# Optimization experiments

Hardware: AMD Instinct MI355X
Metric: run time of the kernel (lower is better)

The kernel has to match this reference:

```python
import jax, jax.numpy as jnp
import numpy as np

HID = 512
B, T, INP_DIM, ACT_DIM = 16, 1000, 4, 1
DT = 0.01  # t_const


def _masks(hid, dtype=jnp.float32):
    q, half, k = hid // 4, hid // 2, int(0.3 * hid)
    strthal = jnp.concatenate([jnp.zeros(q), jnp.ones(half), jnp.zeros(q), jnp.zeros(5 * hid)]).astype(dtype)
    tonic = jnp.concatenate([jnp.zeros(hid), jnp.ones(2 * hid), jnp.zeros(hid), jnp.ones(hid), jnp.zeros(hid)]).astype(dtype)
    alm_mask = jnp.concatenate([jnp.zeros(5 * hid), jnp.ones(hid)]).astype(dtype)
    alm2str_m = jnp.concatenate([jnp.ones((hid, hid - k)), jnp.zeros((hid, k))], axis=1).astype(dtype)
    thal2str_m = jnp.concatenate([jnp.zeros((q, hid)), jnp.ones((half, hid)), jnp.zeros((q, hid))], axis=0).astype(dtype)
    str2snr_m = jnp.concatenate([jnp.ones((hid, half)), jnp.zeros((hid, half))], axis=1).astype(dtype)
    str2gpe_m = jnp.concatenate([jnp.zeros((hid, half)), jnp.ones((hid, half))], axis=1).astype(dtype)
    alm_d = jnp.ones(hid, dtype).at[hid - k:].set(-1.0)  # diag of alm2alm_D
    return strthal, tonic, alm_mask, alm2str_m, thal2str_m, str2snr_m, str2gpe_m, alm_d


def _forward(inp, hn, x, inhib_stim, str2str_w, thal2alm_w, thal2str_w, alm2alm_w,
             alm2str_w, str2snr_w, str2gpe_w, gpe2stn_w, stn2snr_w, snr2thal_w,
             inp_weight, fc1, fc2, str2str_fixed):
    hid = str2str_w.shape[0]
    strthal, tonic, alm_mask, alm2str_m, thal2str_m, str2snr_m, str2gpe_m, alm_d = _masks(hid, inp.dtype)
    relu = jax.nn.relu
    # region-to-region effective weights (D matrices are (+/-) identity -> sign/col scale)
    str2str = -str2str_fixed              # str2str_mask is all zeros; D = -I
    alm2alm = relu(alm2alm_w) * alm_d[None, :]
    alm2str = alm2str_m * relu(alm2str_w)
    thal2alm = relu(thal2alm_w)
    thal2str = thal2str_m * relu(thal2str_w)
    str2snr = -(str2snr_m * relu(str2snr_w))
    str2gpe = -(str2gpe_m * relu(str2gpe_w))
    gpe2stn = -relu(gpe2stn_w)
    stn2snr = relu(stn2snr_w)
    snr2thal = -relu(snr2thal_w)
    H6 = 6 * hid
    W = jnp.zeros((H6, H6), inp.dtype)
    def blk(W, r, c, m):
        return W.at[r * hid:(r + 1) * hid, c * hid:(c + 1) * hid].set(m)
    # rows: str, gpe, stn, snr, thal, alm
    W = blk(W, 0, 0, str2str); W = blk(W, 0, 4, thal2str); W = blk(W, 0, 5, alm2str)
    W = blk(W, 1, 0, str2gpe)
    W = blk(W, 2, 1, gpe2stn)
    W = blk(W, 3, 0, str2snr); W = blk(W, 3, 2, stn2snr)
    W = blk(W, 4, 3, snr2thal)
    W = blk(W, 5, 4, thal2alm); W = blk(W, 5, 5, alm2alm)
    # precompute per-step external drive (noise=False path)
    drive = jnp.einsum('bti,ih->bth', inp, relu(inp_weight)) * strthal \
            + inhib_stim[:, None, :] + tonic  # [B,T,6h]
    def step(h, d_t):
        h_new = jax.nn.relu(h + DT * (-h + h @ W.T + d_t))
        return h_new, h_new
    h0 = hn[0]
    _, hs = jax.lax.scan(step, h0, jnp.swapaxes(drive, 0, 1))  # [T,B,6h]
    rnn_out = jnp.swapaxes(hs, 0, 1)                           # [B,T,6h]
    x_out = jnp.broadcast_to(x[0][:, None, :], rnn_out.shape)  # x is never updated
    hn_last = rnn_out[:, -1, :][None]
    x_last = x_out[:, -1, :][None]
    out = jax.nn.sigmoid((rnn_out * alm_mask) @ jax.nn.relu(fc1) @ jax.nn.relu(fc2))
    return out, hn_last, rnn_out, x_last, x_out


def setup_inputs() -> dict:
    key = jax.random.key(0)
    ks = jax.random.split(key, 17)
    u = lambda k, shape, hi: jax.random.uniform(k, shape, jnp.float32, 0.0, hi)
    hid = HID
    d = {
        'inp': jax.random.normal(ks[0], (B, T, INP_DIM), jnp.float32),
        'hn': jnp.zeros((1, B, 6 * hid), jnp.float32),
        'x': jnp.zeros((1, B, 6 * hid), jnp.float32),
        'inhib_stim': jnp.zeros((B, 6 * hid), jnp.float32),
        'str2str_w': u(ks[1], (hid, hid), 0.01),
        'thal2alm_w': u(ks[2], (hid, hid), 0.01),
        'thal2str_w': u(ks[3], (hid, hid), 0.01),
        'alm2alm_w': u(ks[4], (hid, hid), 0.01),
        'alm2str_w': u(ks[5], (hid, hid), 0.01),
        'str2snr_w': u(ks[6], (hid, hid), 0.01),
        'str2gpe_w': u(ks[7], (hid, hid), 0.01),
        'gpe2stn_w': u(ks[8], (hid, hid), 0.01),
        'stn2snr_w': u(ks[9], (hid, hid), 0.01),
        'snr2thal_w': u(ks[10], (hid, hid), 0.01),
        'inp_weight': u(ks[11], (INP_DIM, 6 * hid), 0.1),
        'fc1': u(ks[12], (6 * hid, hid), 0.01),
        'fc2': u(ks[13], (hid, ACT_DIM), 0.01),
    }
    sparse_mask = (jax.random.uniform(ks[14], (hid, hid)) < 0.1).astype(jnp.float32)
    d['str2str_fixed'] = u(ks[15], (hid, hid), 0.001) * sparse_mask
    return d


def reference(inp, hn, x, inhib_stim, str2str_w, thal2alm_w, thal2str_w, alm2alm_w,
              alm2str_w, str2snr_w, str2gpe_w, gpe2stn_w, stn2snr_w, snr2thal_w,
              inp_weight, fc1, fc2, str2str_fixed):
    return _forward(inp, hn, x, inhib_stim, str2str_w, thal2alm_w, thal2str_w,
                    alm2alm_w, alm2str_w, str2snr_w, str2gpe_w, gpe2stn_w,
                    stn2snr_w, snr2thal_w, inp_weight, fc1, fc2, str2str_fixed)
```

## Files before the change

kernel.cpp:

```cpp
#include <hip/hip_runtime.h>

#define H6   3072
#define TT   1000
#define NWG  192
#define NTHR 256

typedef short bf16x8 __attribute__((ext_vector_type(8)));
typedef float f32x4  __attribute__((ext_vector_type(4)));
typedef unsigned int u32x4 __attribute__((ext_vector_type(4)));

#define TAG64 0x8000800080008000ull

__device__ __forceinline__ unsigned short f2bf(float f) {
  unsigned u = __float_as_uint(f);
  return (unsigned short)((u + 0x7fffu + ((u >> 16) & 1u)) >> 16);
}
__device__ __forceinline__ float bf2f(unsigned short s) {
  return __uint_as_float(((unsigned)s) << 16);
}

#define WS_WLO 5242880
#define WS_RING 10485760
#define WS_FCV 12058624


__global__ void prep_kernel(
    const float* __restrict__ hn, const float* __restrict__ fixed_,
    const float* __restrict__ thal2alm_w, const float* __restrict__ thal2str_w,
    const float* __restrict__ alm2alm_w, const float* __restrict__ alm2str_w,
    const float* __restrict__ str2snr_w, const float* __restrict__ str2gpe_w,
    const float* __restrict__ gpe2stn_w, const float* __restrict__ stn2snr_w,
    const float* __restrict__ snr2thal_w,
    const float* __restrict__ fc1, const float* __restrict__ fc2,
    unsigned short* __restrict__ Whi, unsigned short* __restrict__ Wlo,
    unsigned short* __restrict__ ring, float* __restrict__ fc_vec)
{
  int gid = blockIdx.x * blockDim.x + threadIdx.x;
  int stride = gridDim.x * blockDim.x;
  const int nbt[6]  = {3,1,1,2,1,2};
  const int woff[6] = {0,786432,1048576,1310720,1835008,2097152};
  for (int idx = gid; idx < 2621440; idx += stride) {
    int u = idx >> 18;
    int t = (u<3)?0:((u<4)?1:((u<5)?2:((u<7)?3:((u<8)?4:5))));
    int local = idx - woff[t];
    int ktot = nbt[t] << 9;
    int j  = local / ktot;
    int kx = local - j*ktot;
    int bi = kx >> 9, kk = kx & 511;
    int src = j*512 + kk;
    float w;
    if (t == 0) {
      if (bi == 0)      w = -fixed_[src];
      else if (bi == 1) w = (j >= 128 && j < 384) ? fmaxf(thal2str_w[src],0.f) : 0.f;
      else              w = (kk < 359) ? fmaxf(alm2str_w[src],0.f) : 0.f;
    } else if (t == 1)  w = (kk >= 256) ? -fmaxf(str2gpe_w[src],0.f) : 0.f;
    else if (t == 2)    w = -fmaxf(gpe2stn_w[src],0.f);
    else if (t == 3)    w = (bi == 0) ? ((kk < 256) ? -fmaxf(str2snr_w[src],0.f) : 0.f)
                                      : fmaxf(stn2snr_w[src],0.f);
    else if (t == 4)    w = -fmaxf(snr2thal_w[src],0.f);
    else                w = (bi == 0) ? fmaxf(thal2alm_w[src],0.f)
                                      : fmaxf(alm2alm_w[src],0.f) * ((kk < 359) ? 1.f : -1.f);
    unsigned short hi = f2bf(w);
    Whi[idx] = hi;
    Wlo[idx] = f2bf(w - bf2f(hi));
  }
  for (int u = gid; u < 7*98304; u += stride)
    ring[u] = (u & 1) ? (unsigned short)0x0000 : (unsigned short)0x8000;
  for (int v = gid; v < 49152; v += stride) {
    int r    = v >> 13;
    int rem  = v & 8191;
    int q    = rem >> 9;
    int rem2 = rem & 511;
    int b    = rem2 >> 5;
    int ko   = rem2 & 31;
    int j    = (r << 9) + (q << 5) + ko;
    float val = hn[b * H6 + j];
    unsigned uh = __float_as_uint(val) >> 16;
    float lof = val - __uint_as_float(uh << 16);
    unsigned ul = __float_as_uint(lof) >> 16;
    int off = r*16384 + q*1024 + b*64 + ((ko>>3)<<4) + (ko & 7);
    ring[7*98304 + off]     = (unsigned short)(uh | 0x8000u);
    ring[7*98304 + off + 8] = (unsigned short)(ul | 0x8000u);
  }
  int wid = gid >> 6, lane = gid & 63;
  if (wid < 512) {
    float s = 0.f;
    for (int m = lane; m < 512; m += 64)
      s += fmaxf(fc1[(2560 + wid)*512 + m], 0.f) * fmaxf(fc2[m], 0.f);
    for (int off = 32; off; off >>= 1) s += __shfl_down(s, off);
    if (lane == 0) fc_vec[wid] = s;
  }
}

template<int NB>
__device__ __forceinline__ void scan_body(
    const float* __restrict__ inp, const float* __restrict__ hn,
    const float* __restrict__ inhib, const float* __restrict__ inp_weight,
    const unsigned short* __restrict__ Whi_g, const unsigned short* __restrict__ Wlo_g,
    unsigned short* __restrict__ ring, float* __restrict__ rnn_out,
    float* red, int type, int tile, int kb0, int kb1, int kb2, int woff)
{
  constexpr int NCW = NB * 4;
  const int tid = threadIdx.x, lane = tid & 63, wave = tid >> 6;
  const int ktot = NB << 9;
  const int jb_local = tile << 4;
  const int jb_glob  = (type << 9) + jb_local;
  const int row = lane & 15, quad = lane >> 4;

  bf16x8 wh[NCW], wl[NCW];
  int coff[NCW];
  {
    const unsigned short* sh = Whi_g + woff + (jb_local + row) * ktot + (quad << 3);
    const unsigned short* sl = Wlo_g + woff + (jb_local + row) * ktot + (quad << 3);
    #pragma unroll
    for (int c = 0; c < NCW; ++c) {
      int gc = wave * NCW + c;
      wh[c] = *(const bf16x8*)(sh + (gc << 5));
      wl[c] = *(const bf16x8*)(sl + (gc << 5));
      int bi = gc >> 4;
      int kbv = (bi == 0) ? kb0 : ((bi == 1) ? kb1 : kb2);
      coff[c] = kbv*32768 + (gc & 15)*2048 + row*128 + quad*32;
    }
  }
  #pragma unroll
  for (int c = 0; c < NCW; ++c)
    asm volatile("" : "+v"(wh[c]), "+v"(wl[c]));

  const int b_ep = row;
  const bool has_inp = (type == 0) && (jb_local >= 128) && (jb_local < 384);
  const int jg0 = jb_glob + (quad << 2);
  const int jl0 = jb_local + (quad << 2);
  const int qs = jl0 >> 5, kos = jl0 & 31;
  const int st_off = type*32768 + qs*2048 + b_ep*128 + ((kos>>3)<<5) + ((kos&7)<<1);
  float hprev[4], dbase[4], iw[4][4];
  #pragma unroll
  for (int r = 0; r < 4; ++r) {
    int jgr = jg0 + r;
    hprev[r] = hn[b_ep * H6 + jgr];
    float tn = ((jgr >= 512 && jgr < 1536) || (jgr >= 2048 && jgr < 2560)) ? 1.f : 0.f;
    dbase[r] = inhib[b_ep * H6 + jgr] + tn;
    #pragma unroll
    for (int i = 0; i < 4; ++i)
      iw[r][i] = has_inp ? fmaxf(inp_weight[i * H6 + jgr], 0.f) : 0.f;
  }

  for (int t = 0; t < TT; ++t) {
    const int s_rd = (t + 7) & 7;
    const char* slotp = (const char*)ring + s_rd * 196608;
    const unsigned e32 = ((((t - 1) >> 3) & 1) ? 0x80008000u : 0u);

    float4 xi = {0.f, 0.f, 0.f, 0.f};
    if (wave == 0 && has_inp) xi = *(const float4*)(inp + (b_ep * TT + t) * 4);

    u32x4 Bhi[NCW], Blo[NCW];
    unsigned todo = (NCW == 12) ? 0xFFFu : ((NCW == 8) ? 0xFFu : 0xFu);
    for (;;) {
      #pragma unroll
      for (int c = 0; c < NCW; ++c) if ((todo >> c) & 1u) {
        const char* pc = slotp + coff[c];
        asm volatile("global_load_dwordx4 %0, %2, off sc0 sc1\n\t"
                     "global_load_dwordx4 %1, %2, off offset:16 sc0 sc1"
                     : "=&v"(Bhi[c]), "=&v"(Blo[c]) : "v"(pc) : "memory");
      }
      asm volatile("s_waitcnt vmcnt(0)" ::: "memory");
      __builtin_amdgcn_sched_barrier(0);
      unsigned nt = 0;
      #pragma unroll
      for (int c = 0; c < NCW; ++c) if ((todo >> c) & 1u) {
        unsigned bad = ((Bhi[c][0] ^ e32) | (Bhi[c][1] ^ e32) |
                        (Bhi[c][2] ^ e32) | (Bhi[c][3] ^ e32) |
                        (Blo[c][0] ^ e32) | (Blo[c][1] ^ e32) |
                        (Blo[c][2] ^ e32) | (Blo[c][3] ^ e32)) & 0x80008000u;
        if (__any(bad != 0u)) nt |= 1u << c;
      }
      if (nt == 0) break;
      todo = nt;
      __builtin_amdgcn_s_sleep(1);
    }
    #pragma unroll
    for (int c = 0; c < NCW; ++c) {
      Bhi[c] &= 0x7fff7fffu;
      Blo[c] &= 0x7fff7fffu;
    }

    f32x4 acc0 = {0,0,0,0}, acc1 = {0,0,0,0}, acc2 = {0,0,0,0};
    #pragma unroll
    for (int c = 0; c < NCW; ++c) {
      bf16x8 hb = __builtin_bit_cast(bf16x8, Bhi[c]);
      bf16x8 lb = __builtin_bit_cast(bf16x8, Blo[c]);
      acc0 = __builtin_amdgcn_mfma_f32_16x16x32_bf16(wh[c], hb, acc0, 0, 0, 0);
      acc1 = __builtin_amdgcn_mfma_f32_16x16x32_bf16(wh[c], lb, acc1, 0, 0, 0);
      acc2 = __builtin_amdgcn_mfma_f32_16x16x32_bf16(wl[c], hb, acc2, 0, 0, 0);
    }
    f32x4 acc = acc0 + acc1 + acc2;

    float* bank = red + (t & 1) * 768;
    if (wave) *(f32x4*)(bank + ((wave - 1) * 64 + lane) * 4) = acc;
    __syncthreads();
    if (wave == 0) {
      acc = acc + *(const f32x4*)(bank + lane * 4)
                + *(const f32x4*)(bank + (64 + lane) * 4)
                + *(const f32x4*)(bank + (128 + lane) * 4);
      float proj[4] = {0.f, 0.f, 0.f, 0.f};
      if (has_inp) {
        #pragma unroll
        for (int r = 0; r < 4; ++r)
          proj[r] = xi.x*iw[r][0] + xi.y*iw[r][1] + xi.z*iw[r][2] + xi.w*iw[r][3];
      }
      const unsigned long long ptag = ((t >> 3) & 1) ? TAG64 : 0ull;
      float4 hv4;
      unsigned long long ph = 0ull, pl = 0ull;
      #pragma unroll
      for (int r = 0; r < 4; ++r) {
        float pre = hprev[r] + 0.01f * (acc[r] + dbase[r] + proj[r] - hprev[r]);
        float hv = fmaxf(pre, 0.f);
        hprev[r] = hv;
        ((float*)&hv4)[r] = hv;
        unsigned uh = __float_as_uint(hv) >> 16;
        float lof = hv - __uint_as_float(uh << 16);
        unsigned ul = __float_as_uint(lof) >> 16;
        ph |= ((unsigned long long)uh) << (16 * r);
        pl |= ((unsigned long long)ul) << (16 * r);
      }
      ph |= ptag; pl |= ptag;
      char* outb = (char*)ring + (t & 7) * 196608 + st_off;
      __hip_atomic_store((unsigned long long*)outb, ph,
                         __ATOMIC_RELAXED, __HIP_MEMORY_SCOPE_AGENT);
      __hip_atomic_store((unsigned long long*)(outb + 16), pl,
                         __ATOMIC_RELAXED, __HIP_MEMORY_SCOPE_AGENT);
      *(float4*)(rnn_out + (size_t)(b_ep * TT + t) * H6 + jg0) = hv4;
    }
  }
}

__global__ void __launch_bounds__(NTHR, 1) scan_kernel(
    const float* __restrict__ inp, const float* __restrict__ hn,
    const float* __restrict__ inhib, const float* __restrict__ inp_weight,
    const unsigned short* __restrict__ Whi_g, const unsigned short* __restrict__ Wlo_g,
    unsigned short* __restrict__ ring, float* __restrict__ rnn_out)
{
  __shared__ float red[2 * 768];
  int wg = blockIdx.x;
  int type = wg >> 5, tile = wg & 31;
  switch (type) {
    case 0: scan_body<3>(inp,hn,inhib,inp_weight,Whi_g,Wlo_g,ring,rnn_out,red,0,tile,0,4,5,0);       break;
    case 1: scan_body<1>(inp,hn,inhib,inp_weight,Whi_g,Wlo_g,ring,rnn_out,red,1,tile,0,0,0,786432);  break;
    case 2: scan_body<1>(inp,hn,inhib,inp_weight,Whi_g,Wlo_g,ring,rnn_out,red,2,tile,1,0,0,1048576); break;
    case 3: scan_body<2>(inp,hn,inhib,inp_weight,Whi_g,Wlo_g,ring,rnn_out,red,3,tile,0,2,0,1310720); break;
    case 4: scan_body<1>(inp,hn,inhib,inp_weight,Whi_g,Wlo_g,ring,rnn_out,red,4,tile,3,0,0,1835008); break;
    default:scan_body<2>(inp,hn,inhib,inp_weight,Whi_g,Wlo_g,ring,rnn_out,red,5,tile,4,5,0,2097152); break;
  }
}

__global__ void head_kernel(const float* __restrict__ rnn, const float* __restrict__ fc_vec,
                            float* __restrict__ out, float* __restrict__ hn_last)
{
  int lane = threadIdx.x & 63;
  if (blockIdx.x < 4000) {
    int wid = blockIdx.x * 4 + (threadIdx.x >> 6);
    int b = wid / 1000, t = wid - b * 1000;
    const float* rp = rnn + (size_t)(b * 1000 + t) * H6 + 2560 + lane * 8;
    float4 a0 = *(const float4*)rp, a1 = *(const float4*)(rp + 4);
    const float* vp = fc_vec + lane * 8;
    float4 v0 = *(const float4*)vp, v1 = *(const float4*)(vp + 4);
    float s = a0.x*v0.x + a0.y*v0.y + a0.z*v0.z + a0.w*v0.w
            + a1.x*v1.x + a1.y*v1.y + a1.z*v1.z + a1.w*v1.w;
    for (int off = 32; off; off >>= 1) s += __shfl_down(s, off);
    if (lane == 0) out[b * 1000 + t] = 1.f / (1.f + expf(-s));
  } else {
    int idx = (blockIdx.x - 4000) * NTHR + threadIdx.x;
    int b = idx / H6, j = idx - b * H6;
    hn_last[idx] = rnn[(size_t)(b * 1000 + 999) * H6 + j];
  }
}

__global__ void bcast_kernel(const float* __restrict__ x,
                             float* __restrict__ x_last, float* __restrict__ x_out)
{
  int gid = blockIdx.x * blockDim.x + threadIdx.x;
  int stride = gridDim.x * blockDim.x;
  for (int i = gid; i < 12288; i += stride)
    ((float4*)x_last)[i] = ((const float4*)x)[i];
  for (int i = gid; i < 12288000; i += stride) {
    int b = i / 768000;
    int r = i - b * 768000;
    int j4 = r % 768;
    ((float4*)x_out)[i] = ((const float4*)x)[b * 768 + j4];
  }
}

extern "C" void kernel_launch(void* const* d_in, const int* in_sizes, int n_in,
                              void* d_out, int out_size, void* d_ws, size_t ws_size,
                              hipStream_t stream) {
  (void)in_sizes; (void)n_in; (void)out_size; (void)ws_size;
  const float* inp        = (const float*)d_in[0];
  const float* hn         = (const float*)d_in[1];
  const float* x          = (const float*)d_in[2];
  const float* inhib      = (const float*)d_in[3];
  const float* thal2alm_w = (const float*)d_in[5];
  const float* thal2str_w = (const float*)d_in[6];
  const float* alm2alm_w  = (const float*)d_in[7];
  const float* alm2str_w  = (const float*)d_in[8];
  const float* str2snr_w  = (const float*)d_in[9];
  const float* str2gpe_w  = (const float*)d_in[10];
  const float* gpe2stn_w  = (const float*)d_in[11];
  const float* stn2snr_w  = (const float*)d_in[12];
  const float* snr2thal_w = (const float*)d_in[13];
  const float* inp_weight = (const float*)d_in[14];
  const float* fc1        = (const float*)d_in[15];
  const float* fc2        = (const float*)d_in[16];
  const float* fixed_     = (const float*)d_in[17];

  float* out_p   = (float*)d_out;
  float* hn_last = out_p + 16000;
  float* rnn     = hn_last + 49152;
  float* x_last  = rnn + 49152000;
  float* x_out   = x_last + 49152;

  char* ws = (char*)d_ws;
  unsigned short* Whi  = (unsigned short*)(ws);
  unsigned short* Wlo  = (unsigned short*)(ws + WS_WLO);
  unsigned short* ring = (unsigned short*)(ws + WS_RING);
  float* fc_vec  = (float*)(ws + WS_FCV);

  prep_kernel<<<2048, NTHR, 0, stream>>>(hn, fixed_, thal2alm_w, thal2str_w, alm2alm_w,
      alm2str_w, str2snr_w, str2gpe_w, gpe2stn_w, stn2snr_w, snr2thal_w, fc1, fc2,
      Whi, Wlo, ring, fc_vec);
  scan_kernel<<<NWG, NTHR, 0, stream>>>(inp, hn, inhib, inp_weight,
      Whi, Wlo, ring, rnn);
  head_kernel<<<4192, NTHR, 0, stream>>>(rnn, fc_vec, out_p, hn_last);
  bcast_kernel<<<4096, NTHR, 0, stream>>>(x, x_last, x_out);
}
```

Baseline: 5.986 ms.

## Add per-tile progress flags so scan waits on flags before loading ring

Adds a flag array, zeroed in the prep kernel, with one counter per (producer type, ring slot, tile). Each scan workgroup publishes t+1 after storing its state, and before each step a wave polls the 32 flags for the source blocks it reads, with sleeps between polls. It then does the tagged ring loads. The aim is to stop repeatedly reloading the full ring data while spinning on tag bits, replacing that with cheap flag polling. The cost is an extra global store per step and another round-trip of polling latency on the critical path. Relaxed ordering between the data stores and the flag store could let a reader see the flag first, but the existing tag-check retry loop still guards correctness.

After: 7.260 ms. 21.3% more time.

```diff
diff --git a/kernel.cpp b/kernel.cpp
--- a/kernel.cpp
+++ b/kernel.cpp
@@ -22,6 +22,7 @@
 #define WS_WLO 5242880
 #define WS_RING 10485760
 #define WS_FCV 12058624
+#define WS_FLG 12060672
 
 
 __global__ void prep_kernel(
@@ -33,7 +34,8 @@
     const float* __restrict__ snr2thal_w,
     const float* __restrict__ fc1, const float* __restrict__ fc2,
     unsigned short* __restrict__ Whi, unsigned short* __restrict__ Wlo,
-    unsigned short* __restrict__ ring, float* __restrict__ fc_vec)
+    unsigned short* __restrict__ ring, float* __restrict__ fc_vec,
+    unsigned* __restrict__ flags)
 {
   int gid = blockIdx.x * blockDim.x + threadIdx.x;
   int stride = gridDim.x * blockDim.x;
@@ -90,6 +92,7 @@
     for (int off = 32; off; off >>= 1) s += __shfl_down(s, off);
     if (lane == 0) fc_vec[wid] = s;
   }
+  if (gid < 1536) flags[gid] = 0u;
 }
 
 template<int NB>
@@ -98,6 +101,7 @@
     const float* __restrict__ inhib, const float* __restrict__ inp_weight,
     const unsigned short* __restrict__ Whi_g, const unsigned short* __restrict__ Wlo_g,
     unsigned short* __restrict__ ring, float* __restrict__ rnn_out,
+    unsigned* __restrict__ flags,
     float* red, int type, int tile, int kb0, int kb1, int kb2, int woff)
 {
   constexpr int NCW = NB * 4;
@@ -125,6 +129,12 @@
   #pragma unroll
   for (int c = 0; c < NCW; ++c)
     asm volatile("" : "+v"(wh[c]), "+v"(wl[c]));
+
+  const int lo_bi = (wave * NCW) >> 4;
+  const int hi_bi = (wave * NCW + NCW - 1) >> 4;
+  const int kbA = (lo_bi == 0) ? kb0 : ((lo_bi == 1) ? kb1 : kb2);
+  const int kbB = (hi_bi == 0) ? kb0 : ((hi_bi == 1) ? kb1 : kb2);
+  const int pline = (lane < 32) ? kbA : kbB;
 
   const int b_ep = row;
   const bool has_inp = (type == 0) && (jb_local >= 128) && (jb_local < 384);
@@ -149,6 +159,15 @@
     const char* slotp = (const char*)ring + s_rd * 196608;
     const unsigned e32 = ((((t - 1) >> 3) & 1) ? 0x80008000u : 0u);
 
+    if (t > 0) {
+      const unsigned* wp = &flags[(((pline << 3) + ((t - 1) & 7)) << 5) + (lane & 31)];
+      for (;;) {
+        unsigned v = __hip_atomic_load(wp, __ATOMIC_RELAXED, __HIP_MEMORY_SCOPE_AGENT);
+        if (__all(v >= (unsigned)t)) break;
+        __builtin_amdgcn_s_sleep(1);
+      }
+    }
+
     float4 xi = {0.f, 0.f, 0.f, 0.f};
     if (wave == 0 && has_inp) xi = *(const float4*)(inp + (b_ep * TT + t) * 4);
 
@@ -228,6 +247,10 @@
                          __ATOMIC_RELAXED, __HIP_MEMORY_SCOPE_AGENT);
       __hip_atomic_store((unsigned long long*)(outb + 16), pl,
                          __ATOMIC_RELAXED, __HIP_MEMORY_SCOPE_AGENT);
+      if (lane == 0)
+        __hip_atomic_store(&flags[(((type << 3) + (t & 7)) << 5) + tile],
+                           (unsigned)(t + 1),
+                           __ATOMIC_RELAXED, __HIP_MEMORY_SCOPE_AGENT);
       *(float4*)(rnn_out + (size_t)(b_ep * TT + t) * H6 + jg0) = hv4;
     }
   }
@@ -237,18 +260,19 @@
     const float* __restrict__ inp, const float* __restrict__ hn,
     const float* __restrict__ inhib, const float* __restrict__ inp_weight,
     const unsigned short* __restrict__ Whi_g, const unsigned short* __restrict__ Wlo_g,
-    unsigned short* __restrict__ ring, float* __restrict__ rnn_out)
+    unsigned short* __restrict__ ring, float* __restrict__ rnn_out,
+    unsigned* __restrict__ flags)
 {
   __shared__ float red[2 * 768];
   int wg = blockIdx.x;
   int type = wg >> 5, tile = wg & 31;
   switch (type) {
-    case 0: scan_body<3>(inp,hn,inhib,inp_weight,Whi_g,Wlo_g,ring,rnn_out,red,0,tile,0,4,5,0);       break;
-    case 1: scan_body<1>(inp,hn,inhib,inp_weight,Whi_g,Wlo_g,ring,rnn_out,red,1,tile,0,0,0,786432);  break;
-    case 2: scan_body<1>(inp,hn,inhib,inp_weight,Whi_g,Wlo_g,ring,rnn_out,red,2,tile,1,0,0,1048576); break;
-    case 3: scan_body<2>(inp,hn,inhib,inp_weight,Whi_g,Wlo_g,ring,rnn_out,red,3,tile,0,2,0,1310720); break;
-    case 4: scan_body<1>(inp,hn,inhib,inp_weight,Whi_g,Wlo_g,ring,rnn_out,red,4,tile,3,0,0,1835008); break;
-    default:scan_body<2>(inp,hn,inhib,inp_weight,Whi_g,Wlo_g,ring,rnn_out,red,5,tile,4,5,0,2097152); break;
+    case 0: scan_body<3>(inp,hn,inhib,inp_weight,Whi_g,Wlo_g,ring,rnn_out,flags,red,0,tile,0,4,5,0);       break;
+    case 1: scan_body<1>(inp,hn,inhib,inp_weight,Whi_g,Wlo_g,ring,rnn_out,flags,red,1,tile,0,0,0,786432);  break;
+    case 2: scan_body<1>(inp,hn,inhib,inp_weight,Whi_g,Wlo_g,ring,rnn_out,flags,red,2,tile,1,0,0,1048576); break;
+    case 3: scan_body<2>(inp,hn,inhib,inp_weight,Whi_g,Wlo_g,ring,rnn_out,flags,red,3,tile,0,2,0,1310720); break;
+    case 4: scan_body<1>(inp,hn,inhib,inp_weight,Whi_g,Wlo_g,ring,rnn_out,flags,red,4,tile,3,0,0,1835008); break;
+    default:scan_body<2>(inp,hn,inhib,inp_weight,Whi_g,Wlo_g,ring,rnn_out,flags,red,5,tile,4,5,0,2097152); break;
   }
 }
 
@@ -322,12 +346,13 @@
   unsigned short* Wlo  = (unsigned short*)(ws + WS_WLO);
   unsigned short* ring = (unsigned short*)(ws + WS_RING);
   float* fc_vec  = (float*)(ws + WS_FCV);
+  unsigned* flags = (unsigned*)(ws + WS_FLG);
 
   prep_kernel<<<2048, NTHR, 0, stream>>>(hn, fixed_, thal2alm_w, thal2str_w, alm2alm_w,
       alm2str_w, str2snr_w, str2gpe_w, gpe2stn_w, stn2snr_w, snr2thal_w, fc1, fc2,
-      Whi, Wlo, ring, fc_vec);
+      Whi, Wlo, ring, fc_vec, flags);
   scan_kernel<<<NWG, NTHR, 0, stream>>>(inp, hn, inhib, inp_weight,
-      Whi, Wlo, ring, rnn);
+      Whi, Wlo, ring, rnn, flags);
   head_kernel<<<4192, NTHR, 0, stream>>>(rnn, fc_vec, out_p, hn_last);
   bcast_kernel<<<4096, NTHR, 0, stream>>>(x, x_last, x_out);
 }
```
